# Kernel optimization log

Hardware: AMD Instinct MI355X
Metric: run time of the kernel (lower is better)

## Reference

```python
import jax, jax.numpy as jnp
import numpy as np


def _binarize(x):
    # sign-binarization with straight-through estimator (matches torch .data trick)
    return x + jax.lax.stop_gradient(jnp.sign(x) - x)


def _conv(x, w):
    # x: NCHW, w: OIHW, stride 1, no padding (padding handled explicitly)
    return jax.lax.conv_general_dilated(
        x, w, window_strides=(1, 1), padding='VALID',
        dimension_numbers=('NCHW', 'OIHW', 'NCHW'))


def _hardtanh(x):
    return jnp.clip(x, -1.0, 1.0)


def _maxpool2(x):
    # 2x2 max pool, stride 2, over spatial dims of NCHW
    return jax.lax.reduce_window(
        x, -jnp.inf, jax.lax.max,
        window_dimensions=(1, 1, 2, 2), window_strides=(1, 1, 2, 2),
        padding='VALID')


def setup_inputs() -> dict:
    key = jax.random.key(0)
    kx, k1, k2, k3, k4 = jax.random.split(key, 5)
    x = jax.random.normal(kx, (32, 3, 512, 512), dtype=jnp.float32)
    w1 = jax.random.normal(k1, (8, 3, 3, 3), dtype=jnp.float32) * 0.1
    w2 = jax.random.normal(k2, (16, 8, 3, 3), dtype=jnp.float32) * 0.1
    w3 = jax.random.normal(k3, (32, 16, 3, 3), dtype=jnp.float32) * 0.1
    w4 = jax.random.normal(k4, (2, 32, 3, 3), dtype=jnp.float32) * 0.1
    return {'x': x, 'w1': w1, 'w2': w2, 'w3': w3, 'w4': w4}


def reference(x, w1, w2, w3, w4):
    # p0: ConstantPad2d(1, value=1)
    h = jnp.pad(x, ((0, 0), (0, 0), (1, 1), (1, 1)), constant_values=1.0)
    # features1: BinarizeConv2d(3,8) -- input has 3 channels so NOT binarized;
    # weights are sign-binarized. Then Hardtanh, MaxPool2d(2,2).
    h = _maxpool2(_hardtanh(_conv(h, _binarize(w1))))          # [B,8,256,256]
    # features2..4: binarize activations (C != 3) and weights, conv, hardtanh
    h = _hardtanh(_conv(_binarize(h), _binarize(w2)))          # [B,16,254,254]
    h = _hardtanh(_conv(_binarize(h), _binarize(w3)))          # [B,32,252,252]
    h = _hardtanh(_conv(_binarize(h), _binarize(w4)))          # [B,2,250,250]
    return h.reshape(h.shape[0], -1)                           # [B, 125000]
```

## Files before the change

kernel.cpp:

```cpp
#include <hip/hip_runtime.h>
#include <hip/hip_bf16.h>
#include <cstdint>


typedef __attribute__((ext_vector_type(2)))  float f32x2;
typedef __attribute__((ext_vector_type(4)))  int int4v;
typedef __attribute__((ext_vector_type(16))) int int16v;

#define WOFF_W2M 0
#define WOFF_W3M 10240
#define WOFF_W4M 20480
#define WOFF_W1D 30720
#define WEIGHTS_BYTES 32768

#define A1_PB (2*256*256*4)
#define A2_PB (254*254*4*4)

__device__ __forceinline__ int fsign(float w) {
    return (w > 0.f) ? 1 : ((w < 0.f) ? -1 : 0);
}

__device__ __forceinline__ void pkfma_lo(f32x2& acc, f32x2 w, f32x2 v) {
    asm("v_pk_fma_f32 %0, %1, %2, %0 op_sel:[0,0,0] op_sel_hi:[1,0,1]"
        : "+v"(acc) : "s"(w), "v"(v));
}
__device__ __forceinline__ void pkfma_hi(f32x2& acc, f32x2 w, f32x2 v) {
    asm("v_pk_fma_f32 %0, %1, %2, %0 op_sel:[0,1,0] op_sel_hi:[1,1,1]"
        : "+v"(acc) : "s"(w), "v"(v));
}

__global__ __launch_bounds__(256) void kprep(const float* __restrict__ w1,
                                             const float* __restrict__ w2,
                                             const float* __restrict__ w3,
                                             const float* __restrict__ w4,
                                             int* __restrict__ w2m,
                                             int* __restrict__ w3m,
                                             int* __restrict__ w4m,
                                             f32x2* __restrict__ w1d) {
    int tid = threadIdx.x;
    int b = blockIdx.x;
    if (b == 0) {
        for (int idx = tid; idx < 576; idx += 256) {
            int t = idx / 64, l = idx % 64;
            int oc = l & 31, icb = (l >> 5) * 16;
            int wd[4] = {0, 0, 0, 0};
            for (int j = 0; j < 16; ++j) {
                int ic = icb + j;
                int s = (oc < 16 && ic < 8) ? fsign(w2[(oc * 8 + ic) * 9 + t]) : 0;
                wd[j >> 2] |= (s & 0xff) << (8 * (j & 3));
            }
            w2m[idx * 4 + 0] = wd[0]; w2m[idx * 4 + 1] = wd[1];
            w2m[idx * 4 + 2] = wd[2]; w2m[idx * 4 + 3] = wd[3];
        }
    } else if (b == 1) {
        for (int idx = tid; idx < 576; idx += 256) {
            int t = idx / 64, l = idx % 64;
            int oc = l & 31, icb = (l >> 5) * 16;
            int wd[4] = {0, 0, 0, 0};
            for (int j = 0; j < 16; ++j) {
                int ic = icb + j;
                int s = (ic < 16) ? fsign(w3[(oc * 16 + ic) * 9 + t]) : 0;
                wd[j >> 2] |= (s & 0xff) << (8 * (j & 3));
            }
            w3m[idx * 4 + 0] = wd[0]; w3m[idx * 4 + 1] = wd[1];
            w3m[idx * 4 + 2] = wd[2]; w3m[idx * 4 + 3] = wd[3];
        }
    } else {
        for (int idx = tid; idx < 576; idx += 256) {
            int t = idx / 64, l = idx % 64;
            int oc = l & 31, icb = (l >> 5) * 16;
            int wd[4] = {0, 0, 0, 0};
            for (int j = 0; j < 16; ++j) {
                int ic = icb + j;
                int s = (oc < 2) ? fsign(w4[(oc * 32 + ic) * 9 + t]) : 0;
                wd[j >> 2] |= (s & 0xff) << (8 * (j & 3));
            }
            w4m[idx * 4 + 0] = wd[0]; w4m[idx * 4 + 1] = wd[1];
            w4m[idx * 4 + 2] = wd[2]; w4m[idx * 4 + 3] = wd[3];
        }
        for (int i = tid; i < 128; i += 256) {
            int op = i / 32, t = i % 32;
            f32x2 pr = {0.f, 0.f};
            if (t < 27) {
                float wa = w1[(2 * op) * 27 + t];
                float wbv = w1[(2 * op + 1) * 27 + t];
                pr[0] = (wa > 0.f) ? 1.f : ((wa < 0.f) ? -1.f : 0.f);
                pr[1] = (wbv > 0.f) ? 1.f : ((wbv < 0.f) ? -1.f : 0.f);
            }
            w1d[i] = pr;
        }
    }
}

__global__ __launch_bounds__(128, 4) void k1(const float* __restrict__ x,
                                             const f32x2* __restrict__ w1d,
                                             uint32_t* __restrict__ a1, int n0) {
    int tx = threadIdx.x;
    int oy = blockIdx.y;
    int ln = blockIdx.z;
    const float* xn = x + (size_t)(n0 + ln) * 3 * 512 * 512;

    int iy0 = 2 * oy - 1;
    int xb  = 4 * tx;

    f32x2 P[3][4][3];

    if (oy > 0 && oy < 255 && tx > 0 && tx < 127) {
#pragma unroll
        for (int ic = 0; ic < 3; ++ic) {
            const float* xc = xn + (size_t)ic * 512 * 512;
#pragma unroll
            for (int r = 0; r < 4; ++r) {
                const float* rp = xc + (size_t)(iy0 + r) * 512 + xb;
                float  lft = rp[-1];
                float4 m   = *(const float4*)rp;
                float  rgt = rp[4];
                P[ic][r][0] = (f32x2){lft, m.x};
                P[ic][r][1] = (f32x2){m.y, m.z};
                P[ic][r][2] = (f32x2){m.w, rgt};
            }
        }
    } else {
        for (int ic = 0; ic < 3; ++ic) {
            const float* xc = xn + (size_t)ic * 512 * 512;
#pragma unroll
            for (int r = 0; r < 4; ++r) {
                int iy = iy0 + r;
                bool yok = ((unsigned)iy < 512u);
                float t[6];
#pragma unroll
                for (int c = 0; c < 6; ++c) {
                    int ix = xb - 1 + c;
                    t[c] = (yok && ((unsigned)ix < 512u))
                               ? xc[(size_t)iy * 512 + ix] : 1.0f;
                }
                P[ic][r][0] = (f32x2){t[0], t[1]};
                P[ic][r][1] = (f32x2){t[2], t[3]};
                P[ic][r][2] = (f32x2){t[4], t[5]};
            }
        }
    }

#define PKTAP(ACC, ROW, COL)                                         \
    do {                                                             \
        if (((COL) & 1) == 0) pkfma_lo(ACC, ww, P[ic][ROW][(COL) >> 1]); \
        else                  pkfma_hi(ACC, ww, P[ic][ROW][(COL) >> 1]); \
    } while (0)

    uint64_t dallA = 0, dallB = 0;
#pragma unroll 1
    for (int op = 0; op < 4; ++op) {
        const f32x2* wb = w1d + op * 32;
        f32x2 wop[27];
#pragma unroll
        for (int t = 0; t < 27; ++t) wop[t] = wb[t];

        f32x2 aA00 = {0.f, 0.f}, aA01 = {0.f, 0.f};
        f32x2 aA10 = {0.f, 0.f}, aA11 = {0.f, 0.f};
        f32x2 aB00 = {0.f, 0.f}, aB01 = {0.f, 0.f};
        f32x2 aB10 = {0.f, 0.f}, aB11 = {0.f, 0.f};
#pragma unroll
        for (int ky = 0; ky < 3; ++ky) {
#pragma unroll
            for (int kx = 0; kx < 3; ++kx) {
#pragma unroll
                for (int ic = 0; ic < 3; ++ic) {
                    f32x2 ww = wop[ic * 9 + ky * 3 + kx];
                    PKTAP(aA00, ky + 0, kx + 0);
                    PKTAP(aA01, ky + 0, kx + 1);
                    PKTAP(aA10, ky + 1, kx + 0);
                    PKTAP(aA11, ky + 1, kx + 1);
                    PKTAP(aB00, ky + 0, kx + 2);
                    PKTAP(aB01, ky + 0, kx + 3);
                    PKTAP(aB10, ky + 1, kx + 2);
                    PKTAP(aB11, ky + 1, kx + 3);
                }
            }
        }
        float mA0 = fmaxf(fmaxf(aA00[0], aA01[0]), fmaxf(aA10[0], aA11[0]));
        float mA1 = fmaxf(fmaxf(aA00[1], aA01[1]), fmaxf(aA10[1], aA11[1]));
        float mB0 = fmaxf(fmaxf(aB00[0], aB01[0]), fmaxf(aB10[0], aB11[0]));
        float mB1 = fmaxf(fmaxf(aB00[1], aB01[1]), fmaxf(aB10[1], aB11[1]));
        int sA0 = (mA0 > 0.f) ? 1 : ((mA0 < 0.f) ? -1 : 0);
        int sA1 = (mA1 > 0.f) ? 1 : ((mA1 < 0.f) ? -1 : 0);
        int sB0 = (mB0 > 0.f) ? 1 : ((mB0 < 0.f) ? -1 : 0);
        int sB1 = (mB1 > 0.f) ? 1 : ((mB1 < 0.f) ? -1 : 0);
        dallA |= (uint64_t)(uint32_t)(sA0 & 0xff) << (8 * (2 * op));
        dallA |= (uint64_t)(uint32_t)(sA1 & 0xff) << (8 * (2 * op + 1));
        dallB |= (uint64_t)(uint32_t)(sB0 & 0xff) << (8 * (2 * op));
        dallB |= (uint64_t)(uint32_t)(sB1 & 0xff) << (8 * (2 * op + 1));
    }
#undef PKTAP

    size_t base = (((size_t)ln * 2) * 256 + oy) * 256 + 2 * tx;
    uint2 v0, v1;
    v0.x = (uint32_t)dallA;         v0.y = (uint32_t)dallB;
    v1.x = (uint32_t)(dallA >> 32); v1.y = (uint32_t)(dallB >> 32);
    *(uint2*)(a1 + base)             = v0;
    *(uint2*)(a1 + base + 256 * 256) = v1;
}

__global__ __launch_bounds__(256) void kconv2(const uint32_t* __restrict__ ain,
                                              const int* __restrict__ wm,
                                              uint32_t* __restrict__ aout) {
    __shared__ uint32_t stb[10][36][2];
    int w    = threadIdx.x >> 6;
    int lane = threadIdx.x & 63;
    int x0 = blockIdx.x * 32;
    int y0 = blockIdx.y * 8;
    int ln = blockIdx.z;

    const int4v* wmv = (const int4v*)wm;
    int4v bfr[9];
#pragma unroll
    for (int t = 0; t < 9; ++t) bfr[t] = wmv[t * 64 + lane];

    const uint32_t* abase = ain + (size_t)ln * 2 * 256 * 256;
    for (int idx = threadIdx.x; idx < 10 * 36 * 2; idx += 256) {
        int icg = idx & 1;
        int r2 = idx >> 1;
        int xx = r2 % 36, row = r2 / 36;
        int gy = y0 + row, gx = x0 + xx;
        uint32_t val = 0;
        if (xx < 34 && gx < 256 && gy < 256)
            val = abase[((size_t)icg * 256 + gy) * 256 + gx];
        stb[row][xx][icg] = val;
    }
    __syncthreads();

    int xl = lane & 31;
    int h  = lane >> 5;
    uint32_t* obase = aout + (size_t)ln * 254 * 254 * 4;

#pragma unroll
    for (int ry = 0; ry < 2; ++ry) {
        int yy = y0 + 2 * w + ry;
        int16v acc = {};
#pragma unroll
        for (int ky = 0; ky < 3; ++ky) {
#pragma unroll
            for (int kx = 0; kx < 3; ++kx) {
                uint32_t d0 = stb[2 * w + ry + ky][xl + kx][0];
                uint32_t d1 = stb[2 * w + ry + ky][xl + kx][1];
                int4v a; a[0] = (int)d0; a[1] = (int)d1; a[2] = 0; a[3] = 0;
                acc = __builtin_amdgcn_mfma_i32_32x32x32_i8(bfr[ky * 3 + kx], a, acc, 0, 0, 0);
            }
        }
        bool ok = (yy < 254) && (x0 + xl < 254);
#pragma unroll
        for (int g = 0; g < 2; ++g) {
            int ocg = 2 * g + h;
            if (ok) {
                uint32_t dw = 0;
#pragma unroll
                for (int j = 0; j < 4; ++j) {
                    int v = min(max(acc[4 * g + j], -1), 1);
                    dw |= (uint32_t)(v & 0xff) << (8 * j);
                }
                obase[((size_t)yy * 254 + x0 + xl) * 4 + ocg] = dw;
            }
        }
    }
}

__global__ __launch_bounds__(256) void kconv34(const uint32_t* __restrict__ a2,
                                               const int* __restrict__ w3m,
                                               const int* __restrict__ w4m,
                                               float* __restrict__ out, int n0) {
    __shared__ uint32_t sA2[12][68][4];
    __shared__ uint32_t sA3[10 * 66 * 9];
    int w    = threadIdx.x >> 6;
    int lane = threadIdx.x & 63;
    int xl = lane & 31;
    int h  = lane >> 5;
    int x0 = blockIdx.x * 62;
    int y0 = blockIdx.y * 8;
    int ln = blockIdx.z;

    const int4v* wmv3 = (const int4v*)w3m;
    int4v bfr[9];
#pragma unroll
    for (int t = 0; t < 9; ++t) bfr[t] = wmv3[t * 64 + lane];

    const uint32_t* abase = a2 + (size_t)ln * 254 * 254 * 4;
    for (int idx = threadIdx.x; idx < 12 * 64 * 4; idx += 256) {
        int row = idx >> 8;
        int xx  = (idx >> 2) & 63;
        int icg = idx & 3;
        int gy = y0 + row, gx = x0 + xx;
        uint32_t val = 0;
        if (gy < 254 && gx < 254)
            val = abase[((size_t)gy * 254 + gx) * 4 + icg];
        sA2[row][xx][icg] = val;
    }
    if (threadIdx.x < 96) {
        int row = threadIdx.x >> 3;
        int xx  = 64 + ((threadIdx.x >> 2) & 1);
        int icg = threadIdx.x & 3;
        int gy = y0 + row, gx = x0 + xx;
        uint32_t val = 0;
        if (gy < 254 && gx < 254)
            val = abase[((size_t)gy * 254 + gx) * 4 + icg];
        sA2[row][xx][icg] = val;
    }
    __syncthreads();

#pragma unroll
    for (int t5 = 0; t5 < 5; ++t5) {
        int t = t5 * 4 + w;
        int row = t >> 1, ct = t & 1;
        int16v acc = {};
#pragma unroll
        for (int ky = 0; ky < 3; ++ky) {
#pragma unroll
            for (int kx = 0; kx < 3; ++kx) {
                int4v a = *(const int4v*)&sA2[row + ky][ct * 32 + xl + kx][0];
                acc = __builtin_amdgcn_mfma_i32_32x32x32_i8(bfr[ky * 3 + kx], a, acc, 0, 0, 0);
            }
        }
        int pbase = (row * 66 + ct * 32 + xl) * 9;
#pragma unroll
        for (int g = 0; g < 4; ++g) {
            uint32_t dw = 0;
#pragma unroll
            for (int j = 0; j < 4; ++j) {
                int v = min(max(acc[4 * g + j], -1), 1);
                dw |= (uint32_t)(v & 0xff) << (8 * j);
            }
            sA3[pbase + 2 * g + h] = dw;
        }
    }

    const int4v* wmv4 = (const int4v*)w4m;
    int4v bf4[9];
#pragma unroll
    for (int t = 0; t < 9; ++t) bf4[t] = wmv4[t * 64 + lane];
    __syncthreads();

    size_t gn = (size_t)(n0 + ln);
#pragma unroll
    for (int t4 = 0; t4 < 4; ++t4) {
        int t = t4 * 4 + w;
        int y = t >> 1, ct2 = t & 1;
        int gy = y0 + y;
        int16v acc = {};
#pragma unroll
        for (int ky = 0; ky < 3; ++ky) {
#pragma unroll
            for (int kx = 0; kx < 3; ++kx) {
                const uint32_t* pb = &sA3[((y + ky) * 66 + ct2 * 32 + xl + kx) * 9 + h * 4];
                int4v bv;
                bv[0] = (int)pb[0]; bv[1] = (int)pb[1];
                bv[2] = (int)pb[2]; bv[3] = (int)pb[3];
                acc = __builtin_amdgcn_mfma_i32_32x32x32_i8(bf4[ky * 3 + kx], bv, acc, 0, 0, 0);
            }
        }
        if (h == 0) {
            int lx = ct2 * 32 + xl;
            if (lx < 62 && x0 + lx < 250 && gy < 250) {
                float v0 = fminf(fmaxf((float)acc[0], -1.f), 1.f);
                float v1 = fminf(fmaxf((float)acc[1], -1.f), 1.f);
                out[((gn * 2 + 0) * 250 + gy) * 250 + x0 + lx] = v0;
                out[((gn * 2 + 1) * 250 + gy) * 250 + x0 + lx] = v1;
            }
        }
    }
}

extern "C" void kernel_launch(void* const* d_in, const int* in_sizes, int n_in,
                              void* d_out, int out_size, void* d_ws, size_t ws_size,
                              hipStream_t stream) {
    const float* x  = (const float*)d_in[0];
    const float* w1 = (const float*)d_in[1];
    const float* w2 = (const float*)d_in[2];
    const float* w3 = (const float*)d_in[3];
    const float* w4 = (const float*)d_in[4];
    char* ws = (char*)d_ws;

    int*   w2m = (int*)(ws + WOFF_W2M);
    int*   w3m = (int*)(ws + WOFF_W3M);
    int*   w4m = (int*)(ws + WOFF_W4M);
    f32x2* w1d = (f32x2*)(ws + WOFF_W1D);
    float* out = (float*)d_out;

    size_t per = (size_t)A1_PB + (size_t)A2_PB;
    int NC = 32;
    while (NC > 1 && (size_t)WEIGHTS_BYTES + (size_t)NC * per > ws_size) NC >>= 1;

    uint32_t* A1 = (uint32_t*)(ws + WEIGHTS_BYTES);
    uint32_t* A2 = (uint32_t*)(ws + WEIGHTS_BYTES + (size_t)NC * A1_PB);

    kprep<<<dim3(3), 256, 0, stream>>>(w1, w2, w3, w4, w2m, w3m, w4m, w1d);
    for (int n0 = 0; n0 < 32; n0 += NC) {
        k1<<<dim3(1, 256, NC), 128, 0, stream>>>(x, w1d, A1, n0);
        kconv2<<<dim3(8, 32, NC), 256, 0, stream>>>(A1, w2m, A2);
        kconv34<<<dim3(5, 32, NC), 256, 0, stream>>>(A2, w3m, w4m, out, n0);
    }
}
```

Baseline: 139.7 us.

## Pack multiple conv taps into each int8 MFMA K-dimension to cut MFMA count

Repacks the binarized conv2 and conv3 weight matrices so that each 32x32x32 int8 MFMA covers several kernel taps in its K dimension instead of one tap with zero padding. conv2 now uses 3 MFMAs per output row instead of 9 (four taps of 8 channels each), and conv3 uses 5 instead of 9 (two taps of 16 channels). Each lane gathers its B operand from the shared-memory window at a tap offset that depends on the lane half. The goal is to drop the wasted zero-padded MFMA work, at the cost of divergent per-lane LDS addressing and a more involved weight layout.

```diff
diff --git a/kernel.cpp b/kernel.cpp
--- a/kernel.cpp
+++ b/kernel.cpp
@@ -40,27 +40,33 @@
     int tid = threadIdx.x;
     int b = blockIdx.x;
     if (b == 0) {
-        for (int idx = tid; idx < 576; idx += 256) {
-            int t = idx / 64, l = idx % 64;
-            int oc = l & 31, icb = (l >> 5) * 16;
+        for (int idx = tid; idx < 3 * 64; idx += 256) {
+            int q = idx / 64, l = idx % 64;
+            int oc = l & 31, hl = l >> 5;
             int wd[4] = {0, 0, 0, 0};
-            for (int j = 0; j < 16; ++j) {
-                int ic = icb + j;
-                int s = (oc < 16 && ic < 8) ? fsign(w2[(oc * 8 + ic) * 9 + t]) : 0;
-                wd[j >> 2] |= (s & 0xff) << (8 * (j & 3));
+            for (int u = 0; u < 2; ++u) {
+                int tap = 4 * q + 2 * hl + u;
+                if (tap > 8) continue;
+                for (int i = 0; i < 8; ++i) {
+                    int s = (oc < 16) ? fsign(w2[(oc * 8 + i) * 9 + tap]) : 0;
+                    int j = 8 * u + i;
+                    wd[j >> 2] |= (s & 0xff) << (8 * (j & 3));
+                }
             }
             w2m[idx * 4 + 0] = wd[0]; w2m[idx * 4 + 1] = wd[1];
             w2m[idx * 4 + 2] = wd[2]; w2m[idx * 4 + 3] = wd[3];
         }
     } else if (b == 1) {
-        for (int idx = tid; idx < 576; idx += 256) {
-            int t = idx / 64, l = idx % 64;
-            int oc = l & 31, icb = (l >> 5) * 16;
+        for (int idx = tid; idx < 5 * 64; idx += 256) {
+            int p = idx / 64, l = idx % 64;
+            int oc = l & 31, hl = l >> 5;
             int wd[4] = {0, 0, 0, 0};
-            for (int j = 0; j < 16; ++j) {
-                int ic = icb + j;
-                int s = (ic < 16) ? fsign(w3[(oc * 16 + ic) * 9 + t]) : 0;
-                wd[j >> 2] |= (s & 0xff) << (8 * (j & 3));
+            int tap = (p < 4) ? (2 * p + hl) : ((hl == 0) ? 8 : -1);
+            if (tap >= 0) {
+                for (int j = 0; j < 16; ++j) {
+                    int s = fsign(w3[(oc * 16 + j) * 9 + tap]);
+                    wd[j >> 2] |= (s & 0xff) << (8 * (j & 3));
+                }
             }
             w3m[idx * 4 + 0] = wd[0]; w3m[idx * 4 + 1] = wd[1];
             w3m[idx * 4 + 2] = wd[2]; w3m[idx * 4 + 3] = wd[3];
@@ -209,11 +215,22 @@
     int x0 = blockIdx.x * 32;
     int y0 = blockIdx.y * 8;
     int ln = blockIdx.z;
+    int xl = lane & 31;
+    int h  = lane >> 5;
 
     const int4v* wmv = (const int4v*)wm;
-    int4v bfr[9];
-#pragma unroll
-    for (int t = 0; t < 9; ++t) bfr[t] = wmv[t * 64 + lane];
+    int4v bq[3];
+#pragma unroll
+    for (int q = 0; q < 3; ++q) bq[q] = wmv[q * 64 + lane];
+
+    int ky0_[3], kx0_[3], ky1_[3], kx1_[3];
+#pragma unroll
+    for (int q = 0; q < 3; ++q) {
+        int t0 = 4 * q + 2 * h; if (t0 > 8) t0 = 8;
+        int t1 = 4 * q + 2 * h + 1; if (t1 > 8) t1 = 8;
+        ky0_[q] = t0 / 3; kx0_[q] = t0 % 3;
+        ky1_[q] = t1 / 3; kx1_[q] = t1 % 3;
+    }
 
     const uint32_t* abase = ain + (size_t)ln * 2 * 256 * 256;
     for (int idx = threadIdx.x; idx < 10 * 36 * 2; idx += 256) {
@@ -228,23 +245,20 @@
     }
     __syncthreads();
 
-    int xl = lane & 31;
-    int h  = lane >> 5;
     uint32_t* obase = aout + (size_t)ln * 254 * 254 * 4;
 
 #pragma unroll
     for (int ry = 0; ry < 2; ++ry) {
         int yy = y0 + 2 * w + ry;
+        int rb = 2 * w + ry;
         int16v acc = {};
 #pragma unroll
-        for (int ky = 0; ky < 3; ++ky) {
-#pragma unroll
-            for (int kx = 0; kx < 3; ++kx) {
-                uint32_t d0 = stb[2 * w + ry + ky][xl + kx][0];
-                uint32_t d1 = stb[2 * w + ry + ky][xl + kx][1];
-                int4v a; a[0] = (int)d0; a[1] = (int)d1; a[2] = 0; a[3] = 0;
-                acc = __builtin_amdgcn_mfma_i32_32x32x32_i8(bfr[ky * 3 + kx], a, acc, 0, 0, 0);
-            }
+        for (int q = 0; q < 3; ++q) {
+            uint2 lo = *(const uint2*)&stb[rb + ky0_[q]][xl + kx0_[q]][0];
+            uint2 hi = *(const uint2*)&stb[rb + ky1_[q]][xl + kx1_[q]][0];
+            int4v bv; bv[0] = (int)lo.x; bv[1] = (int)lo.y;
+            bv[2] = (int)hi.x; bv[3] = (int)hi.y;
+            acc = __builtin_amdgcn_mfma_i32_32x32x32_i8(bq[q], bv, acc, 0, 0, 0);
         }
         bool ok = (yy < 254) && (x0 + xl < 254);
 #pragma unroll
@@ -278,9 +292,16 @@
     int ln = blockIdx.z;
 
     const int4v* wmv3 = (const int4v*)w3m;
-    int4v bfr[9];
-#pragma unroll
-    for (int t = 0; t < 9; ++t) bfr[t] = wmv3[t * 64 + lane];
+    int4v bp[5];
+#pragma unroll
+    for (int p = 0; p < 5; ++p) bp[p] = wmv3[p * 64 + lane];
+
+    int kyP[5], kxP[5];
+#pragma unroll
+    for (int p = 0; p < 5; ++p) {
+        int t = (p < 4) ? (2 * p + h) : 8;
+        kyP[p] = t / 3; kxP[p] = t % 3;
+    }
 
     const uint32_t* abase = a2 + (size_t)ln * 254 * 254 * 4;
     for (int idx = threadIdx.x; idx < 12 * 64 * 4; idx += 256) {
@@ -311,12 +332,9 @@
         int row = t >> 1, ct = t & 1;
         int16v acc = {};
 #pragma unroll
-        for (int ky = 0; ky < 3; ++ky) {
-#pragma unroll
-            for (int kx = 0; kx < 3; ++kx) {
-                int4v a = *(const int4v*)&sA2[row + ky][ct * 32 + xl + kx][0];
-                acc = __builtin_amdgcn_mfma_i32_32x32x32_i8(bfr[ky * 3 + kx], a, acc, 0, 0, 0);
-            }
+        for (int p = 0; p < 5; ++p) {
+            int4v a = *(const int4v*)&sA2[row + kyP[p]][ct * 32 + xl + kxP[p]][0];
+            acc = __builtin_amdgcn_mfma_i32_32x32x32_i8(bp[p], a, acc, 0, 0, 0);
         }
         int pbase = (row * 66 + ct * 32 + xl) * 9;
 #pragma unroll
```

Measured after the change: 126.2 us. -9.6%, faster.
